# Performance work log

Hardware: AMD Instinct MI355X
Metric: run time of the kernel (lower is better)

The kernel has to match this reference:

```python
import jax, jax.numpy as jnp
import numpy as np

B = 4096
N_COL = 100      # all-numerical columns
N_COND = 64      # d*m = 4*16
D = 4
TOTAL = N_COL * N_COND   # 6400
N_RODT = TOTAL // D      # 1600
N_EST = 160              # max(2,int(sqrt(100))) * N_COND // D
N_FOREST = 100
N_HIDDEN = 128
N_CLASS = 10
EPS = 1e-5


def group_norm(x, w, b, groups):
    # x: [B, C] (spatial dim of 1 dropped); normalize within each channel group
    Bn, C = x.shape
    xg = x.reshape(Bn, groups, C // groups)
    mu = xg.mean(-1, keepdims=True)
    var = ((xg - mu) ** 2).mean(-1, keepdims=True)
    xn = ((xg - mu) * jax.lax.rsqrt(var + EPS)).reshape(Bn, C)
    return xn * w + b


def layer_norm(x, w, b):
    mu = x.mean(-1, keepdims=True)
    var = ((x - mu) ** 2).mean(-1, keepdims=True)
    return (x - mu) * jax.lax.rsqrt(var + EPS) * w + b


def setup_inputs() -> dict:
    key = jax.random.key(0)
    ks = jax.random.split(key, 16)
    s = 0.3  # weight scale
    x = jax.random.normal(ks[0], (B, N_COL), jnp.float32)
    w1 = jax.random.normal(ks[1], (N_COL, N_COND), jnp.float32) * s
    b1 = jax.random.normal(ks[2], (N_COL, N_COND), jnp.float32) * s
    perm = jax.random.permutation(ks[3], TOTAL)
    gn1_w = jnp.ones((TOTAL,), jnp.float32)
    gn1_b = jnp.zeros((TOTAL,), jnp.float32)
    conv2_w = jax.random.normal(ks[4], (N_RODT, D, D), jnp.float32) * s
    conv2_b = jax.random.normal(ks[5], (TOTAL,), jnp.float32) * s
    gn2_w = jnp.ones((TOTAL,), jnp.float32)
    gn2_b = jnp.zeros((TOTAL,), jnp.float32)
    conv3_w = jax.random.normal(ks[6], (N_RODT, D, 1), jnp.float32) * s
    conv3_b = jax.random.normal(ks[7], (N_RODT,), jnp.float32) * s
    # sample-without-replacement per forest (eval-mode fixed indices)
    swr = jax.vmap(lambda k: jax.random.permutation(k, N_RODT)[:N_EST])(
        jax.random.split(ks[8], N_FOREST))
    E = jax.random.normal(ks[9], (N_RODT, N_HIDDEN), jnp.float32)
    ln1_w = jnp.ones((N_HIDDEN,), jnp.float32)
    ln1_b = jnp.zeros((N_HIDDEN,), jnp.float32)
    fc1_w = jax.random.normal(ks[10], (N_HIDDEN, N_HIDDEN), jnp.float32) * (1.0 / np.sqrt(N_HIDDEN))
    fc1_b = jnp.zeros((N_HIDDEN,), jnp.float32)
    ln2_w = jnp.ones((N_HIDDEN,), jnp.float32)
    ln2_b = jnp.zeros((N_HIDDEN,), jnp.float32)
    fc2_w = jax.random.normal(ks[11], (N_HIDDEN, N_CLASS), jnp.float32) * (1.0 / np.sqrt(N_HIDDEN))
    fc2_b = jnp.zeros((N_CLASS,), jnp.float32)
    return dict(x=x, w1=w1, b1=b1, perm=perm, gn1_w=gn1_w, gn1_b=gn1_b,
                conv2_w=conv2_w, conv2_b=conv2_b, gn2_w=gn2_w, gn2_b=gn2_b,
                conv3_w=conv3_w, conv3_b=conv3_b, swr=swr, E=E,
                ln1_w=ln1_w, ln1_b=ln1_b, fc1_w=fc1_w, fc1_b=fc1_b,
                ln2_w=ln2_w, ln2_b=ln2_b, fc2_w=fc2_w, fc2_b=fc2_b)


def reference(x, w1, b1, perm, gn1_w, gn1_b, conv2_w, conv2_b, gn2_w, gn2_b,
              conv3_w, conv3_b, swr, E, ln1_w, ln1_b, fc1_w, fc1_b,
              ln2_w, ln2_b, fc2_w, fc2_b):
    b = x.shape[0]
    # --- ConditionGeneration (numerical path): per-column 1->n_cond group conv + sigmoid
    M = jax.nn.sigmoid(x[:, :, None] * w1[None] + b1[None])        # [B, n_col, n_cond]
    M = M.transpose(0, 2, 1)                                        # [B, n_cond, n_col]
    # --- rODTConstruction: flatten + fixed permutation
    O = M.reshape(b, -1)[:, perm]                                   # [B, total]
    # --- phi_2: GN -> grouped 4->4 conv -> ReLU -> GN -> grouped 4->1 conv
    h = group_norm(O, gn1_w, gn1_b, N_RODT)
    h = jnp.einsum('bgi,gio->bgo', h.reshape(b, N_RODT, D), conv2_w).reshape(b, TOTAL) + conv2_b
    h = jax.nn.relu(h)
    h = group_norm(h, gn2_w, gn2_b, N_RODT)
    w = jnp.einsum('bgi,gio->bgo', h.reshape(b, N_RODT, D), conv3_w)[..., 0] + conv3_b  # [B, n_rodt] (n_head=1)
    # --- rODT forest: gather estimators, softmax over estimators, weighted sum of rODT embeddings
    ws = jax.nn.softmax(w[:, swr], axis=2)                          # [B, n_forest, n_est]
    Ep = E[swr]                                                     # [n_forest, n_est, n_hidden]
    F = jnp.einsum('bfe,fed->bfd', ws, Ep)                          # [B, n_forest, n_hidden]
    # --- bagging MLP (dropout=0)
    h2 = layer_norm(F, ln1_w, ln1_b)
    h2 = jax.nn.relu(h2 @ fc1_w + fc1_b)
    h2 = layer_norm(h2, ln2_w, ln2_b)
    y_hat = h2 @ fc2_w + fc2_b                                      # [B, n_forest, n_class]
    return y_hat.mean(1)                                            # [B, n_class]
```

## Files before the change

### kernel.cpp

```cpp
#include <hip/hip_runtime.h>
#include <hip/hip_bf16.h>
#include <stdint.h>

#define NB 4096
#define NCOL 100
#define NCOND 64
#define NTOTAL 6400
#define NRODT 1600
#define NEST 160
#define NFOR 100
#define NHID 128
#define NCLS 10
#define GEPS 1e-5f

typedef __attribute__((ext_vector_type(8))) short short8;
typedef __attribute__((ext_vector_type(4))) float floatx4;

__device__ __forceinline__ unsigned f2bfu(float x) {
  union { float f; unsigned u; } v; v.f = x;
  return (v.u + 0x8000u) >> 16;
}
__device__ __forceinline__ float bf2f(unsigned short u) {
  union { unsigned u; float f; } v; v.u = ((unsigned)u) << 16;
  return v.f;
}

__device__ __forceinline__ float rowsum16(float v) {
  union { float f; int i; } a, t;
  a.f = v;
  t.i = __builtin_amdgcn_update_dpp(0, a.i, 0x128, 0xf, 0xf, true); a.f += t.f;
  t.i = __builtin_amdgcn_update_dpp(0, a.i, 0x124, 0xf, 0xf, true); a.f += t.f;
  t.i = __builtin_amdgcn_update_dpp(0, a.i, 0x122, 0xf, 0xf, true); a.f += t.f;
  t.i = __builtin_amdgcn_update_dpp(0, a.i, 0x121, 0xf, 0xf, true); a.f += t.f;
  return a.f;
}

__global__ __launch_bounds__(256) void k01_prep(
    const float* __restrict__ x, const float* __restrict__ w1,
    const float* __restrict__ b1, const int* __restrict__ perm,
    const float* __restrict__ gn1w, const float* __restrict__ gn1b,
    const float* __restrict__ c2w, const float* __restrict__ c2b,
    const float* __restrict__ gn2w, const float* __restrict__ gn2b,
    const float* __restrict__ c3w, const float* __restrict__ c3b,
    const float* __restrict__ E, const int* __restrict__ swr,
    const float* __restrict__ fc1w, const float* __restrict__ fc2w,
    unsigned short* __restrict__ wT,
    unsigned short* __restrict__ Bf, unsigned short* __restrict__ W1f,
    unsigned short* __restrict__ W2f, float* __restrict__ out)
{
  __shared__ float xl[64 * NCOL];
  __shared__ int ridx[NEST];
  const int tid = threadIdx.x;
  const int blk = blockIdx.x;

  if (blk < 1600) {
    const int b0 = (blk & 63) * 64;
    const int g  = (blk >> 6) * 64 + (tid >> 2);
    const int i4 = tid & 3;
    for (int i = tid; i < 64 * NCOL; i += 256)
      xl[i] = x[(size_t)b0 * NCOL + i];
    __syncthreads();

    const int4 p4 = *(const int4*)(perm + 4 * g);
    const int pv[4] = {p4.x, p4.y, p4.z, p4.w};
    float w1v[4], b1v[4];
    int pc[4];
#pragma unroll
    for (int i = 0; i < 4; i++) {
      unsigned p = (unsigned)pv[i];
      unsigned j = p / 100u;
      unsigned cc = p - j * 100u;
      pc[i] = (int)cc;
      w1v[i] = w1[cc * NCOND + j];
      b1v[i] = b1[cc * NCOND + j];
    }
    const float4 g1w = *(const float4*)(gn1w + 4 * g);
    const float4 g1b = *(const float4*)(gn1b + 4 * g);
    const float4 cw0 = *(const float4*)(c2w + 16 * g);
    const float4 cw1 = *(const float4*)(c2w + 16 * g + 4);
    const float4 cw2 = *(const float4*)(c2w + 16 * g + 8);
    const float4 cw3 = *(const float4*)(c2w + 16 * g + 12);
    const float4 cbv = *(const float4*)(c2b + 4 * g);
    const float4 g2w = *(const float4*)(gn2w + 4 * g);
    const float4 g2b = *(const float4*)(gn2b + 4 * g);
    const float4 c3v = *(const float4*)(c3w + 4 * g);
    const float c3bv = c3b[g];

    for (int k = 0; k < 4; k++) {
      float v4[4];
#pragma unroll
      for (int j = 0; j < 4; j++) {
        const int bb = k * 16 + i4 * 4 + j;
        float O[4];
#pragma unroll
        for (int i = 0; i < 4; i++) {
          float a = xl[bb * NCOL + pc[i]] * w1v[i] + b1v[i];
          O[i] = 1.0f / (1.0f + __expf(-a));
        }
        float mu = 0.25f * (O[0] + O[1] + O[2] + O[3]);
        float d[4], var = 0.f;
#pragma unroll
        for (int i = 0; i < 4; i++) { d[i] = O[i] - mu; var += d[i] * d[i]; }
        float rs = rsqrtf(0.25f * var + GEPS);
        float xn0 = d[0] * rs * g1w.x + g1b.x;
        float xn1 = d[1] * rs * g1w.y + g1b.y;
        float xn2 = d[2] * rs * g1w.z + g1b.z;
        float xn3 = d[3] * rs * g1w.w + g1b.w;
        float h[4];
        h[0] = xn0*cw0.x + xn1*cw1.x + xn2*cw2.x + xn3*cw3.x + cbv.x;
        h[1] = xn0*cw0.y + xn1*cw1.y + xn2*cw2.y + xn3*cw3.y + cbv.y;
        h[2] = xn0*cw0.z + xn1*cw1.z + xn2*cw2.z + xn3*cw3.z + cbv.z;
        h[3] = xn0*cw0.w + xn1*cw1.w + xn2*cw2.w + xn3*cw3.w + cbv.w;
#pragma unroll
        for (int i = 0; i < 4; i++) h[i] = fmaxf(h[i], 0.f);
        float mu2 = 0.25f * (h[0] + h[1] + h[2] + h[3]);
        float e[4], var2 = 0.f;
#pragma unroll
        for (int i = 0; i < 4; i++) { e[i] = h[i] - mu2; var2 += e[i] * e[i]; }
        float rs2 = rsqrtf(0.25f * var2 + GEPS);
        float hn0 = e[0] * rs2 * g2w.x + g2b.x;
        float hn1 = e[1] * rs2 * g2w.y + g2b.y;
        float hn2 = e[2] * rs2 * g2w.z + g2b.z;
        float hn3 = e[3] * rs2 * g2w.w + g2b.w;
        v4[j] = hn0*c3v.x + hn1*c3v.y + hn2*c3v.z + hn3*c3v.w + c3bv;
      }
      uint2 pk;
      pk.x = f2bfu(v4[0]) | (f2bfu(v4[1]) << 16);
      pk.y = f2bfu(v4[2]) | (f2bfu(v4[3]) << 16);
      *(uint2*)(wT + (size_t)g * NB + b0 + k * 16 + i4 * 4) = pk;
    }
  } else if (blk < 1600 + NFOR) {
    const int fblk = blk - 1600;
    if (tid < NEST) ridx[tid] = swr[fblk * NEST + tid];
    __syncthreads();
    for (int m = tid; m < 2560; m += 256) {
      int lane = m & 63, rest = m >> 6;
      int kc = rest % 5, n = rest / 5;
      int q = lane >> 4, c = lane & 15;
      int e0 = kc * 32 + q * 8;
      int h = n * 16 + c;
      union { unsigned short v[8]; uint4 u; } t;
#pragma unroll
      for (int j = 0; j < 8; j++)
        t.v[j] = (unsigned short)f2bfu(E[(size_t)ridx[e0 + j] * NHID + h]);
      *(uint4*)(Bf + (size_t)fblk * 20480 + (size_t)m * 8) = t.u;
    }
  } else if (blk == 1600 + NFOR) {
    for (int m = tid; m < 2048; m += 256) {
      int lane = m & 63, rest = m >> 6;
      int kc = rest & 3, n = rest >> 2;
      int q = lane >> 4, c = lane & 15;
      int k0 = kc * 32 + q * 8;
      int o = n * 16 + c;
      union { unsigned short v[8]; uint4 u; } t;
#pragma unroll
      for (int j = 0; j < 8; j++)
        t.v[j] = (unsigned short)f2bfu(fc1w[(size_t)(k0 + j) * NHID + o]);
      *(uint4*)(W1f + (size_t)m * 8) = t.u;
    }
  } else if (blk == 1601 + NFOR) {
    for (int m = tid; m < 256; m += 256) {
      int lane = m & 63, kc = m >> 6;
      int q = lane >> 4, c = lane & 15;
      int k0 = kc * 32 + q * 8;
      union { unsigned short v[8]; uint4 u; } t;
#pragma unroll
      for (int j = 0; j < 8; j++)
        t.v[j] = (unsigned short)f2bfu(c < NCLS ? fc2w[(size_t)(k0 + j) * NCLS + c] : 0.f);
      *(uint4*)(W2f + (size_t)m * 8) = t.u;
    }
  } else {
    const int z = blk - (1602 + NFOR);
    float4 zz = make_float4(0.f, 0.f, 0.f, 0.f);
    for (int i = z * 256 + tid; i < NB * NCLS / 4; i += 3 * 256)
      ((float4*)out)[i] = zz;
  }
}

__global__ __launch_bounds__(256, 6) void k3_mfma(
    const unsigned short* __restrict__ wT,
    const int* __restrict__ swr,
    const unsigned short* __restrict__ Bf,
    const unsigned short* __restrict__ W1f,
    const unsigned short* __restrict__ W2f,
    const float* __restrict__ ln1w, const float* __restrict__ ln1b,
    const float* __restrict__ fc1b,
    const float* __restrict__ ln2w, const float* __restrict__ ln2b,
    const float* __restrict__ fc2b,
    float* __restrict__ out)
{
  __shared__ unsigned short lsA[64 * 168];
  __shared__ __align__(16) float sPT[64][4];

  const int tid = threadIdx.x;
  const int b0 = blockIdx.x * 64;
  const int f  = blockIdx.y;
  const int lane = tid & 63;
  const int wv = __builtin_amdgcn_readfirstlane(tid >> 6);
  const int c = lane & 15, q = lane >> 4;

  {
    const unsigned short* wbase = wT + b0 + lane;
    const int* swf = swr + f * NEST + wv * 40;
    float ssum = 0.f;
#pragma unroll
    for (int k = 0; k < 5; k++) {
      int id8[8];
#pragma unroll
      for (int jj = 0; jj < 8; jj++) id8[jj] = swf[k * 8 + jj];
      unsigned us[8];
#pragma unroll
      for (int jj = 0; jj < 8; jj++) {
        float v = bf2f(wbase[(size_t)id8[jj] * NB]);
        float ex = __expf(v);
        ssum += ex;
        us[jj] = f2bfu(ex);
      }
      uint4 pk = {us[0] | (us[1] << 16), us[2] | (us[3] << 16),
                  us[4] | (us[5] << 16), us[6] | (us[7] << 16)};
      *(uint4*)(lsA + lane * 168 + wv * 40 + k * 8) = pk;
    }
    sPT[lane][wv] = ssum;
  }
  __syncthreads();

  const unsigned short* pa = lsA + (wv * 16 + c) * 168 + q * 8;
  floatx4 acc[8];
#pragma unroll
  for (int n = 0; n < 8; n++) acc[n] = (floatx4){0.f, 0.f, 0.f, 0.f};

  const unsigned short* bbase = Bf + (size_t)f * 20480 + lane * 8;
#pragma unroll
  for (int kc = 0; kc < 5; kc++) {
    short8 a = *(const short8*)(pa + kc * 32);
#pragma unroll
    for (int n = 0; n < 8; n++) {
      short8 b = *(const short8*)(bbase + n * 2560 + kc * 512);
      acc[n] = __builtin_amdgcn_mfma_f32_16x16x32_bf16(a, b, acc[n], 0, 0, 0);
    }
  }

  {
    float lw[8], lb[8];
#pragma unroll
    for (int n = 0; n < 8; n++) { lw[n] = ln1w[n * 16 + c]; lb[n] = ln1b[n * 16 + c]; }
#pragma unroll
    for (int rr = 0; rr < 4; rr++) {
      const int row = wv * 16 + q * 4 + rr;
      const float4 sv = *(const float4*)&sPT[row][0];
      float st = sv.x + sv.y + sv.z + sv.w;
      float s1 = 0.f, s2 = 0.f;
#pragma unroll
      for (int n = 0; n < 8; n++) { float v = acc[n][rr]; s1 += v; s2 += v * v; }
      s1 = rowsum16(s1);
      s2 = rowsum16(s2);
      float mu = s1 * (1.f / 128.f);
      float var = fmaxf(s2 * (1.f / 128.f) - mu * mu, 0.f);
      float rs = rsqrtf(var + GEPS * st * st);
#pragma unroll
      for (int n = 0; n < 8; n++)
        acc[n][rr] = (acc[n][rr] - mu) * rs * lw[n] + lb[n];
    }
  }

#pragma unroll
  for (int rr = 0; rr < 4; rr++)
#pragma unroll
    for (int n = 0; n < 8; n++)
      lsA[(wv * 16 + q * 4 + rr) * 168 + n * 16 + c] =
          (unsigned short)f2bfu(acc[n][rr]);

  {
    short8 a0 = *(const short8*)(pa);
    short8 a1 = *(const short8*)(pa + 32);
    short8 a2 = *(const short8*)(pa + 64);
    short8 a3 = *(const short8*)(pa + 96);
#pragma unroll
    for (int n = 0; n < 8; n++) acc[n] = (floatx4){0.f, 0.f, 0.f, 0.f};
    const unsigned short* w1p = W1f + lane * 8;
#pragma unroll
    for (int n = 0; n < 8; n++) {
      const unsigned short* wp = w1p + n * 2048;
      acc[n] = __builtin_amdgcn_mfma_f32_16x16x32_bf16(a0, *(const short8*)(wp),        acc[n], 0, 0, 0);
      acc[n] = __builtin_amdgcn_mfma_f32_16x16x32_bf16(a1, *(const short8*)(wp + 512),  acc[n], 0, 0, 0);
      acc[n] = __builtin_amdgcn_mfma_f32_16x16x32_bf16(a2, *(const short8*)(wp + 1024), acc[n], 0, 0, 0);
      acc[n] = __builtin_amdgcn_mfma_f32_16x16x32_bf16(a3, *(const short8*)(wp + 1536), acc[n], 0, 0, 0);
    }
  }

  {
    float fb[8], lw[8], lb[8];
#pragma unroll
    for (int n = 0; n < 8; n++) {
      fb[n] = fc1b[n * 16 + c];
      lw[n] = ln2w[n * 16 + c]; lb[n] = ln2b[n * 16 + c];
    }
#pragma unroll
    for (int rr = 0; rr < 4; rr++) {
#pragma unroll
      for (int n = 0; n < 8; n++) acc[n][rr] = fmaxf(acc[n][rr] + fb[n], 0.f);
      float s1 = 0.f, s2 = 0.f;
#pragma unroll
      for (int n = 0; n < 8; n++) { float v = acc[n][rr]; s1 += v; s2 += v * v; }
      s1 = rowsum16(s1);
      s2 = rowsum16(s2);
      float mu = s1 * (1.f / 128.f);
      float var = fmaxf(s2 * (1.f / 128.f) - mu * mu, 0.f);
      float rs = rsqrtf(var + GEPS);
#pragma unroll
      for (int n = 0; n < 8; n++)
        acc[n][rr] = (acc[n][rr] - mu) * rs * lw[n] + lb[n];
    }
  }

#pragma unroll
  for (int rr = 0; rr < 4; rr++)
#pragma unroll
    for (int n = 0; n < 8; n++)
      lsA[(wv * 16 + q * 4 + rr) * 168 + n * 16 + c] =
          (unsigned short)f2bfu(acc[n][rr]);

  floatx4 o4 = (floatx4){0.f, 0.f, 0.f, 0.f};
#pragma unroll
  for (int kc = 0; kc < 4; kc++) {
    short8 a = *(const short8*)(pa + kc * 32);
    short8 b = *(const short8*)(W2f + kc * 512 + lane * 8);
    o4 = __builtin_amdgcn_mfma_f32_16x16x32_bf16(a, b, o4, 0, 0, 0);
  }
  if (c < NCLS) {
    float bias = fc2b[c];
#pragma unroll
    for (int rr = 0; rr < 4; rr++)
      atomicAdd(out + (size_t)(b0 + wv * 16 + q * 4 + rr) * NCLS + c,
                (o4[rr] + bias) * 0.01f);
  }
}

extern "C" void kernel_launch(void* const* d_in, const int* in_sizes, int n_in,
                              void* d_out, int out_size, void* d_ws, size_t ws_size,
                              hipStream_t stream)
{
  (void)in_sizes; (void)n_in; (void)ws_size; (void)out_size;
  const float* x    = (const float*)d_in[0];
  const float* w1   = (const float*)d_in[1];
  const float* b1   = (const float*)d_in[2];
  const int*   perm = (const int*)d_in[3];
  const float* gn1w = (const float*)d_in[4];
  const float* gn1b = (const float*)d_in[5];
  const float* c2w  = (const float*)d_in[6];
  const float* c2b  = (const float*)d_in[7];
  const float* gn2w = (const float*)d_in[8];
  const float* gn2b = (const float*)d_in[9];
  const float* c3w  = (const float*)d_in[10];
  const float* c3b  = (const float*)d_in[11];
  const int*   swr  = (const int*)d_in[12];
  const float* E    = (const float*)d_in[13];
  const float* ln1w = (const float*)d_in[14];
  const float* ln1b = (const float*)d_in[15];
  const float* fc1w = (const float*)d_in[16];
  const float* fc1b = (const float*)d_in[17];
  const float* ln2w = (const float*)d_in[18];
  const float* ln2b = (const float*)d_in[19];
  const float* fc2w = (const float*)d_in[20];
  const float* fc2b = (const float*)d_in[21];
  float* out = (float*)d_out;

  const size_t W_BYTES = (size_t)NB * NRODT * 2;
  unsigned short* wTbuf = (unsigned short*)d_ws;
  unsigned short* Bfb   = (unsigned short*)((char*)d_ws + W_BYTES);
  unsigned short* W1fb  = (unsigned short*)((char*)d_ws + W_BYTES + 4096000);
  unsigned short* W2fb  = (unsigned short*)((char*)d_ws + W_BYTES + 4096000 + 32768);

  k01_prep<<<1600 + NFOR + 2 + 3, 256, 0, stream>>>(
      x, w1, b1, perm, gn1w, gn1b, c2w, c2b, gn2w, gn2b, c3w, c3b,
      E, swr, fc1w, fc2w, wTbuf, Bfb, W1fb, W2fb, out);
  dim3 g3(NB / 64, NFOR);
  k3_mfma<<<g3, 256, 0, stream>>>(wTbuf, swr, Bfb, W1fb, W2fb,
                                  ln1w, ln1b, fc1b, ln2w, ln2b, fc2b, out);
}
```

Baseline: 219.7 us.

## Precompute exp in prep kernel and process four forests per block

```diff
diff --git a/kernel.cpp b/kernel.cpp
--- a/kernel.cpp
+++ b/kernel.cpp
@@ -125,8 +125,8 @@
         v4[j] = hn0*c3v.x + hn1*c3v.y + hn2*c3v.z + hn3*c3v.w + c3bv;
       }
       uint2 pk;
-      pk.x = f2bfu(v4[0]) | (f2bfu(v4[1]) << 16);
-      pk.y = f2bfu(v4[2]) | (f2bfu(v4[3]) << 16);
+      pk.x = f2bfu(__expf(v4[0])) | (f2bfu(__expf(v4[1])) << 16);
+      pk.y = f2bfu(__expf(v4[2])) | (f2bfu(__expf(v4[3])) << 16);
       *(uint2*)(wT + (size_t)g * NB + b0 + k * 16 + i4 * 4) = pk;
     }
   } else if (blk < 1600 + NFOR) {
@@ -194,145 +194,155 @@
 
   const int tid = threadIdx.x;
   const int b0 = blockIdx.x * 64;
-  const int f  = blockIdx.y;
+  const int f0 = blockIdx.y * 4;
   const int lane = tid & 63;
   const int wv = __builtin_amdgcn_readfirstlane(tid >> 6);
   const int c = lane & 15, q = lane >> 4;
 
-  {
-    const unsigned short* wbase = wT + b0 + lane;
-    const int* swf = swr + f * NEST + wv * 40;
-    float ssum = 0.f;
-#pragma unroll
-    for (int k = 0; k < 5; k++) {
-      int id8[8];
-#pragma unroll
-      for (int jj = 0; jj < 8; jj++) id8[jj] = swf[k * 8 + jj];
-      unsigned us[8];
-#pragma unroll
-      for (int jj = 0; jj < 8; jj++) {
-        float v = bf2f(wbase[(size_t)id8[jj] * NB]);
-        float ex = __expf(v);
-        ssum += ex;
-        us[jj] = f2bfu(ex);
-      }
-      uint4 pk = {us[0] | (us[1] << 16), us[2] | (us[3] << 16),
-                  us[4] | (us[5] << 16), us[6] | (us[7] << 16)};
-      *(uint4*)(lsA + lane * 168 + wv * 40 + k * 8) = pk;
-    }
-    sPT[lane][wv] = ssum;
+  const unsigned short* pa = lsA + (wv * 16 + c) * 168 + q * 8;
+  floatx4 oacc = (floatx4){0.f, 0.f, 0.f, 0.f};
+
+#pragma unroll 1
+  for (int fi = 0; fi < 4; fi++) {
+    const int f = f0 + fi;
+    if (fi) __syncthreads();
+
+    {
+      const unsigned short* wbase = wT + b0 + lane;
+      const int* swf = swr + f * NEST + wv * 40;
+      float ssum = 0.f;
+#pragma unroll
+      for (int k = 0; k < 5; k++) {
+        int id8[8];
+#pragma unroll
+        for (int jj = 0; jj < 8; jj++) id8[jj] = swf[k * 8 + jj];
+        unsigned short us[8];
+#pragma unroll
+        for (int jj = 0; jj < 8; jj++) {
+          us[jj] = wbase[(size_t)id8[jj] * NB];
+          ssum += bf2f(us[jj]);
+        }
+        uint4 pk = {(unsigned)us[0] | ((unsigned)us[1] << 16),
+                    (unsigned)us[2] | ((unsigned)us[3] << 16),
+                    (unsigned)us[4] | ((unsigned)us[5] << 16),
+                    (unsigned)us[6] | ((unsigned)us[7] << 16)};
+        *(uint4*)(lsA + lane * 168 + wv * 40 + k * 8) = pk;
+      }
+      sPT[lane][wv] = ssum;
+    }
+    __syncthreads();
+
+    floatx4 acc[8];
+#pragma unroll
+    for (int n = 0; n < 8; n++) acc[n] = (floatx4){0.f, 0.f, 0.f, 0.f};
+
+    const unsigned short* bbase = Bf + (size_t)f * 20480 + lane * 8;
+#pragma unroll
+    for (int kc = 0; kc < 5; kc++) {
+      short8 a = *(const short8*)(pa + kc * 32);
+#pragma unroll
+      for (int n = 0; n < 8; n++) {
+        short8 b = *(const short8*)(bbase + n * 2560 + kc * 512);
+        acc[n] = __builtin_amdgcn_mfma_f32_16x16x32_bf16(a, b, acc[n], 0, 0, 0);
+      }
+    }
+
+    {
+      float lw[8], lb[8];
+#pragma unroll
+      for (int n = 0; n < 8; n++) { lw[n] = ln1w[n * 16 + c]; lb[n] = ln1b[n * 16 + c]; }
+#pragma unroll
+      for (int rr = 0; rr < 4; rr++) {
+        const int row = wv * 16 + q * 4 + rr;
+        const float4 sv = *(const float4*)&sPT[row][0];
+        float st = sv.x + sv.y + sv.z + sv.w;
+        float s1 = 0.f, s2 = 0.f;
+#pragma unroll
+        for (int n = 0; n < 8; n++) { float v = acc[n][rr]; s1 += v; s2 += v * v; }
+        s1 = rowsum16(s1);
+        s2 = rowsum16(s2);
+        float mu = s1 * (1.f / 128.f);
+        float var = fmaxf(s2 * (1.f / 128.f) - mu * mu, 0.f);
+        float rs = rsqrtf(var + GEPS * st * st);
+#pragma unroll
+        for (int n = 0; n < 8; n++)
+          acc[n][rr] = (acc[n][rr] - mu) * rs * lw[n] + lb[n];
+      }
+    }
+
+#pragma unroll
+    for (int rr = 0; rr < 4; rr++)
+#pragma unroll
+      for (int n = 0; n < 8; n++)
+        lsA[(wv * 16 + q * 4 + rr) * 168 + n * 16 + c] =
+            (unsigned short)f2bfu(acc[n][rr]);
+
+    {
+      short8 a0 = *(const short8*)(pa);
+      short8 a1 = *(const short8*)(pa + 32);
+      short8 a2 = *(const short8*)(pa + 64);
+      short8 a3 = *(const short8*)(pa + 96);
+#pragma unroll
+      for (int n = 0; n < 8; n++) acc[n] = (floatx4){0.f, 0.f, 0.f, 0.f};
+      const unsigned short* w1p = W1f + lane * 8;
+#pragma unroll
+      for (int n = 0; n < 8; n++) {
+        const unsigned short* wp = w1p + n * 2048;
+        acc[n] = __builtin_amdgcn_mfma_f32_16x16x32_bf16(a0, *(const short8*)(wp),        acc[n], 0, 0, 0);
+        acc[n] = __builtin_amdgcn_mfma_f32_16x16x32_bf16(a1, *(const short8*)(wp + 512),  acc[n], 0, 0, 0);
+        acc[n] = __builtin_amdgcn_mfma_f32_16x16x32_bf16(a2, *(const short8*)(wp + 1024), acc[n], 0, 0, 0);
+        acc[n] = __builtin_amdgcn_mfma_f32_16x16x32_bf16(a3, *(const short8*)(wp + 1536), acc[n], 0, 0, 0);
+      }
+    }
+
+    {
+      float fb[8], lw[8], lb[8];
+#pragma unroll
+      for (int n = 0; n < 8; n++) {
+        fb[n] = fc1b[n * 16 + c];
+        lw[n] = ln2w[n * 16 + c]; lb[n] = ln2b[n * 16 + c];
+      }
+#pragma unroll
+      for (int rr = 0; rr < 4; rr++) {
+#pragma unroll
+        for (int n = 0; n < 8; n++) acc[n][rr] = fmaxf(acc[n][rr] + fb[n], 0.f);
+        float s1 = 0.f, s2 = 0.f;
+#pragma unroll
+        for (int n = 0; n < 8; n++) { float v = acc[n][rr]; s1 += v; s2 += v * v; }
+        s1 = rowsum16(s1);
+        s2 = rowsum16(s2);
+        float mu = s1 * (1.f / 128.f);
+        float var = fmaxf(s2 * (1.f / 128.f) - mu * mu, 0.f);
+        float rs = rsqrtf(var + GEPS);
+#pragma unroll
+        for (int n = 0; n < 8; n++)
+          acc[n][rr] = (acc[n][rr] - mu) * rs * lw[n] + lb[n];
+      }
+    }
+
+#pragma unroll
+    for (int rr = 0; rr < 4; rr++)
+#pragma unroll
+      for (int n = 0; n < 8; n++)
+        lsA[(wv * 16 + q * 4 + rr) * 168 + n * 16 + c] =
+            (unsigned short)f2bfu(acc[n][rr]);
+
+    floatx4 o4 = (floatx4){0.f, 0.f, 0.f, 0.f};
+#pragma unroll
+    for (int kc = 0; kc < 4; kc++) {
+      short8 a = *(const short8*)(pa + kc * 32);
+      short8 b = *(const short8*)(W2f + kc * 512 + lane * 8);
+      o4 = __builtin_amdgcn_mfma_f32_16x16x32_bf16(a, b, o4, 0, 0, 0);
+    }
+    oacc += o4;
   }
-  __syncthreads();
-
-  const unsigned short* pa = lsA + (wv * 16 + c) * 168 + q * 8;
-  floatx4 acc[8];
-#pragma unroll
-  for (int n = 0; n < 8; n++) acc[n] = (floatx4){0.f, 0.f, 0.f, 0.f};
-
-  const unsigned short* bbase = Bf + (size_t)f * 20480 + lane * 8;
-#pragma unroll
-  for (int kc = 0; kc < 5; kc++) {
-    short8 a = *(const short8*)(pa + kc * 32);
-#pragma unroll
-    for (int n = 0; n < 8; n++) {
-      short8 b = *(const short8*)(bbase + n * 2560 + kc * 512);
-      acc[n] = __builtin_amdgcn_mfma_f32_16x16x32_bf16(a, b, acc[n], 0, 0, 0);
-    }
-  }
-
-  {
-    float lw[8], lb[8];
-#pragma unroll
-    for (int n = 0; n < 8; n++) { lw[n] = ln1w[n * 16 + c]; lb[n] = ln1b[n * 16 + c]; }
-#pragma unroll
-    for (int rr = 0; rr < 4; rr++) {
-      const int row = wv * 16 + q * 4 + rr;
-      const float4 sv = *(const float4*)&sPT[row][0];
-      float st = sv.x + sv.y + sv.z + sv.w;
-      float s1 = 0.f, s2 = 0.f;
-#pragma unroll
-      for (int n = 0; n < 8; n++) { float v = acc[n][rr]; s1 += v; s2 += v * v; }
-      s1 = rowsum16(s1);
-      s2 = rowsum16(s2);
-      float mu = s1 * (1.f / 128.f);
-      float var = fmaxf(s2 * (1.f / 128.f) - mu * mu, 0.f);
-      float rs = rsqrtf(var + GEPS * st * st);
-#pragma unroll
-      for (int n = 0; n < 8; n++)
-        acc[n][rr] = (acc[n][rr] - mu) * rs * lw[n] + lb[n];
-    }
-  }
-
-#pragma unroll
-  for (int rr = 0; rr < 4; rr++)
-#pragma unroll
-    for (int n = 0; n < 8; n++)
-      lsA[(wv * 16 + q * 4 + rr) * 168 + n * 16 + c] =
-          (unsigned short)f2bfu(acc[n][rr]);
-
-  {
-    short8 a0 = *(const short8*)(pa);
-    short8 a1 = *(const short8*)(pa + 32);
-    short8 a2 = *(const short8*)(pa + 64);
-    short8 a3 = *(const short8*)(pa + 96);
-#pragma unroll
-    for (int n = 0; n < 8; n++) acc[n] = (floatx4){0.f, 0.f, 0.f, 0.f};
-    const unsigned short* w1p = W1f + lane * 8;
-#pragma unroll
-    for (int n = 0; n < 8; n++) {
-      const unsigned short* wp = w1p + n * 2048;
-      acc[n] = __builtin_amdgcn_mfma_f32_16x16x32_bf16(a0, *(const short8*)(wp),        acc[n], 0, 0, 0);
-      acc[n] = __builtin_amdgcn_mfma_f32_16x16x32_bf16(a1, *(const short8*)(wp + 512),  acc[n], 0, 0, 0);
-      acc[n] = __builtin_amdgcn_mfma_f32_16x16x32_bf16(a2, *(const short8*)(wp + 1024), acc[n], 0, 0, 0);
-      acc[n] = __builtin_amdgcn_mfma_f32_16x16x32_bf16(a3, *(const short8*)(wp + 1536), acc[n], 0, 0, 0);
-    }
-  }
-
-  {
-    float fb[8], lw[8], lb[8];
-#pragma unroll
-    for (int n = 0; n < 8; n++) {
-      fb[n] = fc1b[n * 16 + c];
-      lw[n] = ln2w[n * 16 + c]; lb[n] = ln2b[n * 16 + c];
-    }
-#pragma unroll
-    for (int rr = 0; rr < 4; rr++) {
-#pragma unroll
-      for (int n = 0; n < 8; n++) acc[n][rr] = fmaxf(acc[n][rr] + fb[n], 0.f);
-      float s1 = 0.f, s2 = 0.f;
-#pragma unroll
-      for (int n = 0; n < 8; n++) { float v = acc[n][rr]; s1 += v; s2 += v * v; }
-      s1 = rowsum16(s1);
-      s2 = rowsum16(s2);
-      float mu = s1 * (1.f / 128.f);
-      float var = fmaxf(s2 * (1.f / 128.f) - mu * mu, 0.f);
-      float rs = rsqrtf(var + GEPS);
-#pragma unroll
-      for (int n = 0; n < 8; n++)
-        acc[n][rr] = (acc[n][rr] - mu) * rs * lw[n] + lb[n];
-    }
-  }
-
-#pragma unroll
-  for (int rr = 0; rr < 4; rr++)
-#pragma unroll
-    for (int n = 0; n < 8; n++)
-      lsA[(wv * 16 + q * 4 + rr) * 168 + n * 16 + c] =
-          (unsigned short)f2bfu(acc[n][rr]);
-
-  floatx4 o4 = (floatx4){0.f, 0.f, 0.f, 0.f};
-#pragma unroll
-  for (int kc = 0; kc < 4; kc++) {
-    short8 a = *(const short8*)(pa + kc * 32);
-    short8 b = *(const short8*)(W2f + kc * 512 + lane * 8);
-    o4 = __builtin_amdgcn_mfma_f32_16x16x32_bf16(a, b, o4, 0, 0, 0);
-  }
+
   if (c < NCLS) {
-    float bias = fc2b[c];
+    float bias4 = 4.f * fc2b[c];
 #pragma unroll
     for (int rr = 0; rr < 4; rr++)
       atomicAdd(out + (size_t)(b0 + wv * 16 + q * 4 + rr) * NCLS + c,
-                (o4[rr] + bias) * 0.01f);
+                (oacc[rr] + bias4) * 0.01f);
   }
 }
 
@@ -374,7 +384,7 @@
   k01_prep<<<1600 + NFOR + 2 + 3, 256, 0, stream>>>(
       x, w1, b1, perm, gn1w, gn1b, c2w, c2b, gn2w, gn2b, c3w, c3b,
       E, swr, fc1w, fc2w, wTbuf, Bfb, W1fb, W2fb, out);
-  dim3 g3(NB / 64, NFOR);
+  dim3 g3(NB / 64, NFOR / 4);
   k3_mfma<<<g3, 256, 0, stream>>>(wTbuf, swr, Bfb, W1fb, W2fb,
                                   ln1w, ln1b, fc1b, ln2w, ln2b, fc2b, out);
 }
```

Result: slower. 638.0 us (+190.4%).
